# Kernel tuning notes

Measured on AMD Instinct MI355X. Metric: run time of the kernel, lower is better.

The kernel has to match this reference:

```python
import jax, jax.numpy as jnp
import numpy as np

DIM = 512
HEADS = 8
HEAD_DIM = DIM // HEADS
SCALE = HEAD_DIM ** -0.5


def setup_inputs() -> dict:
    key = jax.random.key(0)
    k1, k2, k3, k4, k5 = jax.random.split(key, 5)
    x = jax.random.normal(k1, (2, 4096, DIM), dtype=jnp.float32)
    # qkv Linear: weight [3*dim, dim], bias [3*dim]; proj: [dim, dim], [dim]
    w_qkv = jax.random.normal(k2, (3 * DIM, DIM), dtype=jnp.float32) * (DIM ** -0.5)
    b_qkv = jax.random.normal(k3, (3 * DIM,), dtype=jnp.float32) * 0.02
    w_proj = jax.random.normal(k4, (DIM, DIM), dtype=jnp.float32) * (DIM ** -0.5)
    b_proj = jax.random.normal(k5, (DIM,), dtype=jnp.float32) * 0.02
    return {"x": x, "w_qkv": w_qkv, "b_qkv": b_qkv, "w_proj": w_proj, "b_proj": b_proj}


def reference(x, w_qkv, b_qkv, w_proj, b_proj):
    B, N, C = x.shape
    qkv = x @ w_qkv.T + b_qkv  # [B, N, 3C]
    qkv = qkv.reshape(B, N, 3, HEADS, HEAD_DIM).transpose(2, 0, 3, 1, 4)  # [3,B,H,N,hd]
    q, k, v = qkv[0], qkv[1], qkv[2]
    attn = jnp.einsum('bhnd,bhmd->bhnm', q, k) * SCALE  # explicit NxN matrix
    attn = jax.nn.softmax(attn, axis=-1)
    out = jnp.einsum('bhnm,bhmd->bhnd', attn, v)  # [B,H,N,hd]
    out = out.transpose(0, 2, 1, 3).reshape(B, N, C)
    return out @ w_proj.T + b_proj
```

## Files before the change

kernel.cpp:

```cpp
#include <hip/hip_runtime.h>

typedef __bf16 bf16x8 __attribute__((ext_vector_type(8)));
typedef __bf16 bf16x4 __attribute__((ext_vector_type(4)));
typedef __bf16 bf16x2 __attribute__((ext_vector_type(2)));
typedef float  floatx4 __attribute__((ext_vector_type(4)));
typedef unsigned int uint32;
typedef uint32 uintx4 __attribute__((ext_vector_type(4)));

#define MFMA16(a,b,c) __builtin_amdgcn_mfma_f32_16x16x32_bf16(a,b,c,0,0,0)

constexpr int DIM  = 512;
constexpr int SEQ  = 4096;
constexpr int HD   = 64;
constexpr float QSCALE = 0.1803368801111244f;

static __device__ inline __bf16 f2bf(float f) {
    unsigned int u = __builtin_bit_cast(unsigned int, f);
    u += 0x7fffu + ((u >> 16) & 1u);
    return __builtin_bit_cast(__bf16, (unsigned short)(u >> 16));
}
#if __has_builtin(__builtin_amdgcn_cvt_pk_bf16_f32)
static __device__ inline bf16x2 pk2(float a, float b) {
    return __builtin_amdgcn_cvt_pk_bf16_f32(a, b);
}
#else
static __device__ inline bf16x2 pk2(float a, float b) {
    bf16x2 r; r[0] = f2bf(a); r[1] = f2bf(b); return r;
}
#endif
#if __has_builtin(__builtin_amdgcn_exp2f)
#define EXP2(x) __builtin_amdgcn_exp2f(x)
#else
#define EXP2(x) exp2f(x)
#endif
static __device__ inline bf16x8 cvt8(floatx4 lo, floatx4 hi) {
    uintx4 w;
    w[0] = __builtin_bit_cast(uint32, pk2(lo[0], lo[1]));
    w[1] = __builtin_bit_cast(uint32, pk2(lo[2], lo[3]));
    w[2] = __builtin_bit_cast(uint32, pk2(hi[0], hi[1]));
    w[3] = __builtin_bit_cast(uint32, pk2(hi[2], hi[3]));
    return __builtin_bit_cast(bf16x8, w);
}

static __device__ inline void gload16(const __bf16* g, __bf16* l) {
#if __has_builtin(__builtin_amdgcn_global_load_lds)
    __builtin_amdgcn_global_load_lds(
        (const __attribute__((address_space(1))) unsigned int*)g,
        (__attribute__((address_space(3))) unsigned int*)l, 16, 0, 0);
#else
    *(bf16x8*)(l + (threadIdx.x & 63)*8) = *(const bf16x8*)g;
#endif
}


__global__ __launch_bounds__(256)
void gemm_qkv(const float* __restrict__ X, const float* __restrict__ W,
              const float* __restrict__ bias,
              __bf16* __restrict__ Qb, __bf16* __restrict__ Kb, __bf16* __restrict__ Vb)
{
    __shared__ __bf16 As[128*32];
    __shared__ __bf16 Bs[128*32];
    const int tid  = threadIdx.x;
    const int lane = tid & 63;
    const int wave = tid >> 6;
    const int quad = lane >> 4;
    const int l16  = lane & 15;
    const int waveM = wave >> 1, waveN = wave & 1;
    const int mBase = blockIdx.x * 128;
    const int nBase = blockIdx.y * 128;
    const int which = nBase >> 9;

    floatx4 zero = {0.f, 0.f, 0.f, 0.f};
    floatx4 acc[4][4];
    for (int i = 0; i < 4; i++)
        for (int j = 0; j < 4; j++) acc[i][j] = zero;

    const int srow = tid >> 2;
    const int scol = (tid & 3) * 8;

    for (int k0 = 0; k0 < DIM; k0 += 32) {
        const float* xr0 = X + (size_t)(mBase + srow)      * DIM + k0 + scol;
        const float* xr1 = X + (size_t)(mBase + 64 + srow) * DIM + k0 + scol;
        const float* wr0 = W + (size_t)(nBase + srow)      * DIM + k0 + scol;
        const float* wr1 = W + (size_t)(nBase + 64 + srow) * DIM + k0 + scol;
        bf16x8 a0 = cvt8(*(const floatx4*)xr0, *(const floatx4*)(xr0 + 4));
        bf16x8 a1 = cvt8(*(const floatx4*)xr1, *(const floatx4*)(xr1 + 4));
        bf16x8 b0 = cvt8(*(const floatx4*)wr0, *(const floatx4*)(wr0 + 4));
        bf16x8 b1 = cvt8(*(const floatx4*)wr1, *(const floatx4*)(wr1 + 4));
        *(bf16x8*)&As[srow*32 + scol]      = a0;
        *(bf16x8*)&As[(64+srow)*32 + scol] = a1;
        *(bf16x8*)&Bs[srow*32 + scol]      = b0;
        *(bf16x8*)&Bs[(64+srow)*32 + scol] = b1;
        __syncthreads();
        bf16x8 af[4], bfr[4];
        for (int mi = 0; mi < 4; mi++)
            af[mi]  = *(const bf16x8*)&As[(waveM*64 + mi*16 + l16)*32 + quad*8];
        for (int ni = 0; ni < 4; ni++)
            bfr[ni] = *(const bf16x8*)&Bs[(waveN*64 + ni*16 + l16)*32 + quad*8];
        if (which == 2) {
            for (int mi = 0; mi < 4; mi++)
                for (int ni = 0; ni < 4; ni++)
                    acc[mi][ni] = MFMA16(af[mi], bfr[ni], acc[mi][ni]);
        } else {
            for (int mi = 0; mi < 4; mi++)
                for (int ni = 0; ni < 4; ni++)
                    acc[mi][ni] = MFMA16(bfr[ni], af[mi], acc[mi][ni]);
        }
        __syncthreads();
    }

    if (which == 2) {
        for (int ni = 0; ni < 4; ni++) {
            const int n = nBase + waveN*64 + ni*16 + l16;
            const float bv = bias[n];
            const int h = (n >> 6) & 7;
            const int d = n & 63;
            for (int mi = 0; mi < 4; mi++) {
                const int m0 = mBase + waveM*64 + mi*16 + quad*4;
                const int b  = m0 >> 12;
                const int s0 = m0 & 4095;
                const int bh = (b << 3) | h;
                bf16x4 v;
                for (int r = 0; r < 4; r++) v[r] = f2bf(acc[mi][ni][r] + bv);
                size_t off = (((((size_t)bh*128 + (s0 >> 5))*4 + (d >> 4))*64)
                              + ((s0 >> 2) & 3)*16 + (d & 15))*8 + ((s0 >> 4) & 1)*4;
                *(bf16x4*)&Vb[off] = v;
            }
        }
    } else {
        __bf16* dst = (which == 0) ? Qb : Kb;
        for (int ni = 0; ni < 4; ni++) {
            const int n0 = nBase + waveN*64 + ni*16 + quad*4;
            const floatx4 b4 = *(const floatx4*)&bias[n0];
            const int dfull = n0 & 511;
            const int h  = dfull >> 6;
            const int d0 = dfull & 63;
            const int lgrp = ((d0 >> 3) & 3)*16 + l16;
            const int half = d0 >> 5;
            const int slot = d0 & 7;
            for (int mi = 0; mi < 4; mi++) {
                const int m = mBase + waveM*64 + mi*16 + l16;
                const int b = m >> 12, s = m & 4095;
                const int bh = (b << 3) | h;
                bf16x4 v;
                for (int r = 0; r < 4; r++) {
                    float val = acc[mi][ni][r] + b4[r];
                    if (which == 0) val *= QSCALE;
                    v[r] = f2bf(val);
                }
                size_t off = ((((size_t)bh*256 + (s >> 4))*2 + half)*64 + lgrp)*8 + slot;
                *(bf16x4*)&dst[off] = v;
            }
        }
    }
}

__global__ __launch_bounds__(256, 3)
void attn_kernel(const __bf16* __restrict__ Qb, const __bf16* __restrict__ Kb,
                 const __bf16* __restrict__ Vb, __bf16* __restrict__ Ao)
{
    __shared__ __bf16 Ob[3][64*68];
    __shared__ float  Lb[4][64];
    const int tid  = threadIdx.x;
    const int lane = tid & 63;
    const int wave = tid >> 6;
    const int quad = lane >> 4;
    const int l16  = lane & 15;
    const int bh    = blockIdx.x;
    const int qBase = blockIdx.y * 64;

    const __bf16* qg = Qb + (size_t)bh*256*2*512;
    const __bf16* kg = Kb + (size_t)bh*256*2*512;
    const __bf16* vg = Vb + (size_t)bh*128*4*512;

    bf16x8 qf[4][2];
    for (int t = 0; t < 4; t++)
        for (int hb = 0; hb < 2; hb++)
            qf[t][hb] = *(const bf16x8*)(qg
                + ((size_t)((qBase >> 4) + t)*2 + hb)*512 + lane*8);

    floatx4 zero = {0.f, 0.f, 0.f, 0.f};
    floatx4 oacc[4][4];
    for (int t = 0; t < 4; t++)
        for (int od = 0; od < 4; od++) oacc[t][od] = zero;
    floatx4 Lt[4];
    for (int t = 0; t < 4; t++) Lt[t] = zero;

    bf16x8 ones;
    for (int j = 0; j < 8; j++) ones[j] = f2bf(1.0f);

    const int key_begin = wave * 1024;
    const __bf16* kptr = kg + (size_t)(key_begin >> 4)*1024 + lane*8;
    const __bf16* vptr = vg + (size_t)(key_begin >> 5)*2048 + lane*8;

    for (int c = 0; c < 32; ++c) {
        bf16x8 kb00 = *(const bf16x8*)(kptr);
        bf16x8 kb01 = *(const bf16x8*)(kptr + 512);
        bf16x8 kb10 = *(const bf16x8*)(kptr + 1024);
        bf16x8 kb11 = *(const bf16x8*)(kptr + 1536);
        bf16x8 vb0  = *(const bf16x8*)(vptr);
        bf16x8 vb1  = *(const bf16x8*)(vptr + 512);
        bf16x8 vb2  = *(const bf16x8*)(vptr + 1024);
        bf16x8 vb3  = *(const bf16x8*)(vptr + 1536);
        kptr += 2048;
        vptr += 2048;

        for (int t = 0; t < 4; t++) {
            floatx4 z0 = zero, z1 = zero;
            z0 = MFMA16(kb00, qf[t][0], z0);
            z0 = MFMA16(kb01, qf[t][1], z0);
            z1 = MFMA16(kb10, qf[t][0], z1);
            z1 = MFMA16(kb11, qf[t][1], z1);
            float e0[4], e1[4];
            for (int r = 0; r < 4; r++) { e0[r] = EXP2(z0[r]); e1[r] = EXP2(z1[r]); }
            uintx4 w;
            w[0] = __builtin_bit_cast(uint32, pk2(e0[0], e0[1]));
            w[1] = __builtin_bit_cast(uint32, pk2(e0[2], e0[3]));
            w[2] = __builtin_bit_cast(uint32, pk2(e1[0], e1[1]));
            w[3] = __builtin_bit_cast(uint32, pk2(e1[2], e1[3]));
            bf16x8 pb = __builtin_bit_cast(bf16x8, w);
            Lt[t] = MFMA16(ones, pb, Lt[t]);
            oacc[t][0] = MFMA16(vb0, pb, oacc[t][0]);
            oacc[t][1] = MFMA16(vb1, pb, oacc[t][1]);
            oacc[t][2] = MFMA16(vb2, pb, oacc[t][2]);
            oacc[t][3] = MFMA16(vb3, pb, oacc[t][3]);
        }
    }

    if (lane < 16)
        for (int t = 0; t < 4; t++) Lb[wave][t*16 + lane] = Lt[t][0];
    __syncthreads();
    float inv[4];
    for (int t = 0; t < 4; t++) {
        const int q = t*16 + l16;
        inv[t] = 1.0f / (Lb[0][q] + Lb[1][q] + Lb[2][q] + Lb[3][q]);
    }
    if (wave != 0) {
        for (int t = 0; t < 4; t++)
            for (int od = 0; od < 4; od++) {
                bf16x4 v;
                for (int r = 0; r < 4; r++) v[r] = f2bf(oacc[t][od][r] * inv[t]);
                *(bf16x4*)&Ob[wave-1][(t*16 + l16)*68 + od*16 + quad*4] = v;
            }
    }
    __syncthreads();
    if (wave == 0) {
        const int b = bh >> 3, h = bh & 7;
        for (int t = 0; t < 4; t++) {
            const int s = qBase + t*16 + l16;
            for (int od = 0; od < 4; od++) {
                bf16x4 o0 = *(const bf16x4*)&Ob[0][(t*16 + l16)*68 + od*16 + quad*4];
                bf16x4 o1 = *(const bf16x4*)&Ob[1][(t*16 + l16)*68 + od*16 + quad*4];
                bf16x4 o2 = *(const bf16x4*)&Ob[2][(t*16 + l16)*68 + od*16 + quad*4];
                bf16x4 v;
                for (int r = 0; r < 4; r++) {
                    float o = oacc[t][od][r] * inv[t] +
                              (float)o0[r] + (float)o1[r] + (float)o2[r];
                    v[r] = f2bf(o);
                }
                *(bf16x4*)&Ao[((size_t)(b*SEQ + s))*DIM + h*HD + od*16 + quad*4] = v;
            }
        }
    }
}

__global__ __launch_bounds__(256)
void gemm_proj(const __bf16* __restrict__ A, const float* __restrict__ W,
               const float* __restrict__ bias, float* __restrict__ Out)
{
    __shared__ __bf16 As[128*32];
    __shared__ __bf16 Bs[128*32];
    const int tid  = threadIdx.x;
    const int lane = tid & 63;
    const int wave = tid >> 6;
    const int quad = lane >> 4;
    const int l16  = lane & 15;
    const int waveM = wave >> 1, waveN = wave & 1;
    const int mBase = blockIdx.x * 128;
    const int nBase = blockIdx.y * 128;

    floatx4 zero = {0.f, 0.f, 0.f, 0.f};
    floatx4 acc[4][4];
    for (int i = 0; i < 4; i++)
        for (int j = 0; j < 4; j++) acc[i][j] = zero;

    const int srow = tid >> 2;
    const int scol = (tid & 3) * 8;
    const __bf16* gA0 = A + (size_t)(mBase + 32*wave + (lane >> 2))*DIM + (lane & 3)*8;
    __bf16* lA0 = &As[(32*wave)*32];
    __bf16* lA1 = &As[(32*wave + 16)*32];

    for (int k0 = 0; k0 < DIM; k0 += 32) {
        gload16(gA0 + k0,          lA0);
        gload16(gA0 + k0 + 16*DIM, lA1);
        const float* wr0 = W + (size_t)(nBase + srow)      * DIM + k0 + scol;
        const float* wr1 = W + (size_t)(nBase + 64 + srow) * DIM + k0 + scol;
        bf16x8 b0 = cvt8(*(const floatx4*)wr0, *(const floatx4*)(wr0 + 4));
        bf16x8 b1 = cvt8(*(const floatx4*)wr1, *(const floatx4*)(wr1 + 4));
        *(bf16x8*)&Bs[srow*32 + scol]      = b0;
        *(bf16x8*)&Bs[(64+srow)*32 + scol] = b1;
        __syncthreads();
        bf16x8 af[4], bfr[4];
        for (int mi = 0; mi < 4; mi++)
            af[mi]  = *(const bf16x8*)&As[(waveM*64 + mi*16 + l16)*32 + quad*8];
        for (int ni = 0; ni < 4; ni++)
            bfr[ni] = *(const bf16x8*)&Bs[(waveN*64 + ni*16 + l16)*32 + quad*8];
        for (int mi = 0; mi < 4; mi++)
            for (int ni = 0; ni < 4; ni++)
                acc[mi][ni] = MFMA16(af[mi], bfr[ni], acc[mi][ni]);
        __syncthreads();
    }

    for (int ni = 0; ni < 4; ni++) {
        const int n = nBase + waveN*64 + ni*16 + l16;
        const float bv = bias[n];
        for (int mi = 0; mi < 4; mi++) {
            const int m0 = mBase + waveM*64 + mi*16 + quad*4;
            for (int r = 0; r < 4; r++) {
                const int mm = m0 + r;
                Out[(size_t)mm*DIM + n] = acc[mi][ni][r] + bv;
            }
        }
    }
}

extern "C" void kernel_launch(void* const* d_in, const int* in_sizes, int n_in,
                              void* d_out, int out_size, void* d_ws, size_t ws_size,
                              hipStream_t stream) {
    const float* x      = (const float*)d_in[0];
    const float* w_qkv  = (const float*)d_in[1];
    const float* b_qkv  = (const float*)d_in[2];
    const float* w_proj = (const float*)d_in[3];
    const float* b_proj = (const float*)d_in[4];
    float* out = (float*)d_out;

    __bf16* ws  = (__bf16*)d_ws;
    const size_t PLANE = (size_t)16 * SEQ * HD;
    __bf16* Qbk = ws;
    __bf16* Kbk = ws + PLANE;
    __bf16* Vbk = ws + 2*PLANE;
    __bf16* Aob = ws + 3*PLANE;

    gemm_qkv<<<dim3(64, 12), 256, 0, stream>>>(x, w_qkv, b_qkv, Qbk, Kbk, Vbk);
    attn_kernel<<<dim3(16, 64), 256, 0, stream>>>(Qbk, Kbk, Vbk, Aob);
    gemm_proj<<<dim3(64, 4), 256, 0, stream>>>(Aob, w_proj, b_proj, out);
}
```

Before: 229.2 us.

## Double-buffer GEMM tiles, software-pipeline attention K/V loads, shrink proj tiles

The QKV GEMM now uses double-buffered LDS tiles, issuing the next k-slice's global loads before the current MFMAs and storing them afterwards, so each iteration needs one barrier instead of two. The attention kernel prefetches the next K/V chunk into registers while computing the current one, wraps the MFMA groups in s_setprio, and relaxes launch bounds from 3 to 2 waves per SIMD to leave room for the extra registers. The projection GEMM switches to 64x64 double-buffered tiles launched as a 128x8 grid to raise occupancy and parallelism. The cost is more register and LDS use per block, and lower occupancy in attention.

Result: faster. 214.5 us (-6.4%).

```diff
diff --git a/kernel.cpp b/kernel.cpp
--- a/kernel.cpp
+++ b/kernel.cpp
@@ -58,8 +58,8 @@
               const float* __restrict__ bias,
               __bf16* __restrict__ Qb, __bf16* __restrict__ Kb, __bf16* __restrict__ Vb)
 {
-    __shared__ __bf16 As[128*32];
-    __shared__ __bf16 Bs[128*32];
+    __shared__ __bf16 As[2][128*32];
+    __shared__ __bf16 Bs[2][128*32];
     const int tid  = threadIdx.x;
     const int lane = tid & 63;
     const int wave = tid >> 6;
@@ -78,25 +78,38 @@
     const int srow = tid >> 2;
     const int scol = (tid & 3) * 8;
 
-    for (int k0 = 0; k0 < DIM; k0 += 32) {
-        const float* xr0 = X + (size_t)(mBase + srow)      * DIM + k0 + scol;
-        const float* xr1 = X + (size_t)(mBase + 64 + srow) * DIM + k0 + scol;
-        const float* wr0 = W + (size_t)(nBase + srow)      * DIM + k0 + scol;
-        const float* wr1 = W + (size_t)(nBase + 64 + srow) * DIM + k0 + scol;
-        bf16x8 a0 = cvt8(*(const floatx4*)xr0, *(const floatx4*)(xr0 + 4));
-        bf16x8 a1 = cvt8(*(const floatx4*)xr1, *(const floatx4*)(xr1 + 4));
-        bf16x8 b0 = cvt8(*(const floatx4*)wr0, *(const floatx4*)(wr0 + 4));
-        bf16x8 b1 = cvt8(*(const floatx4*)wr1, *(const floatx4*)(wr1 + 4));
-        *(bf16x8*)&As[srow*32 + scol]      = a0;
-        *(bf16x8*)&As[(64+srow)*32 + scol] = a1;
-        *(bf16x8*)&Bs[srow*32 + scol]      = b0;
-        *(bf16x8*)&Bs[(64+srow)*32 + scol] = b1;
-        __syncthreads();
+    const float* xp0 = X + (size_t)(mBase + srow)      * DIM + scol;
+    const float* xp1 = X + (size_t)(mBase + 64 + srow) * DIM + scol;
+    const float* wp0 = W + (size_t)(nBase + srow)      * DIM + scol;
+    const float* wp1 = W + (size_t)(nBase + 64 + srow) * DIM + scol;
+
+    floatx4 r[8];
+    auto LOAD = [&](int k0) {
+        r[0] = *(const floatx4*)(xp0 + k0); r[1] = *(const floatx4*)(xp0 + k0 + 4);
+        r[2] = *(const floatx4*)(xp1 + k0); r[3] = *(const floatx4*)(xp1 + k0 + 4);
+        r[4] = *(const floatx4*)(wp0 + k0); r[5] = *(const floatx4*)(wp0 + k0 + 4);
+        r[6] = *(const floatx4*)(wp1 + k0); r[7] = *(const floatx4*)(wp1 + k0 + 4);
+    };
+    auto STORE = [&](int b) {
+        *(bf16x8*)&As[b][srow*32 + scol]      = cvt8(r[0], r[1]);
+        *(bf16x8*)&As[b][(64+srow)*32 + scol] = cvt8(r[2], r[3]);
+        *(bf16x8*)&Bs[b][srow*32 + scol]      = cvt8(r[4], r[5]);
+        *(bf16x8*)&Bs[b][(64+srow)*32 + scol] = cvt8(r[6], r[7]);
+    };
+
+    LOAD(0);
+    STORE(0);
+    __syncthreads();
+
+    for (int it = 0; it < 16; ++it) {
+        const int cur = it & 1;
+        if (it < 15) LOAD((it + 1) * 32);
+
         bf16x8 af[4], bfr[4];
         for (int mi = 0; mi < 4; mi++)
-            af[mi]  = *(const bf16x8*)&As[(waveM*64 + mi*16 + l16)*32 + quad*8];
+            af[mi]  = *(const bf16x8*)&As[cur][(waveM*64 + mi*16 + l16)*32 + quad*8];
         for (int ni = 0; ni < 4; ni++)
-            bfr[ni] = *(const bf16x8*)&Bs[(waveN*64 + ni*16 + l16)*32 + quad*8];
+            bfr[ni] = *(const bf16x8*)&Bs[cur][(waveN*64 + ni*16 + l16)*32 + quad*8];
         if (which == 2) {
             for (int mi = 0; mi < 4; mi++)
                 for (int ni = 0; ni < 4; ni++)
@@ -106,6 +119,7 @@
                 for (int ni = 0; ni < 4; ni++)
                     acc[mi][ni] = MFMA16(bfr[ni], af[mi], acc[mi][ni]);
         }
+        if (it < 15) STORE(cur ^ 1);
         __syncthreads();
     }
 
@@ -121,7 +135,7 @@
                 const int s0 = m0 & 4095;
                 const int bh = (b << 3) | h;
                 bf16x4 v;
-                for (int r = 0; r < 4; r++) v[r] = f2bf(acc[mi][ni][r] + bv);
+                for (int rr = 0; rr < 4; rr++) v[rr] = f2bf(acc[mi][ni][rr] + bv);
                 size_t off = (((((size_t)bh*128 + (s0 >> 5))*4 + (d >> 4))*64)
                               + ((s0 >> 2) & 3)*16 + (d & 15))*8 + ((s0 >> 4) & 1)*4;
                 *(bf16x4*)&Vb[off] = v;
@@ -143,10 +157,10 @@
                 const int b = m >> 12, s = m & 4095;
                 const int bh = (b << 3) | h;
                 bf16x4 v;
-                for (int r = 0; r < 4; r++) {
-                    float val = acc[mi][ni][r] + b4[r];
+                for (int rr = 0; rr < 4; rr++) {
+                    float val = acc[mi][ni][rr] + b4[rr];
                     if (which == 0) val *= QSCALE;
-                    v[r] = f2bf(val);
+                    v[rr] = f2bf(val);
                 }
                 size_t off = ((((size_t)bh*256 + (s >> 4))*2 + half)*64 + lgrp)*8 + slot;
                 *(bf16x4*)&dst[off] = v;
@@ -155,7 +169,7 @@
     }
 }
 
-__global__ __launch_bounds__(256, 3)
+__global__ __launch_bounds__(256, 2)
 void attn_kernel(const __bf16* __restrict__ Qb, const __bf16* __restrict__ Kb,
                  const __bf16* __restrict__ Vb, __bf16* __restrict__ Ao)
 {
@@ -189,42 +203,54 @@
     bf16x8 ones;
     for (int j = 0; j < 8; j++) ones[j] = f2bf(1.0f);
 
-    const int key_begin = wave * 1024;
-    const __bf16* kptr = kg + (size_t)(key_begin >> 4)*1024 + lane*8;
-    const __bf16* vptr = vg + (size_t)(key_begin >> 5)*2048 + lane*8;
-
-    for (int c = 0; c < 32; ++c) {
-        bf16x8 kb00 = *(const bf16x8*)(kptr);
-        bf16x8 kb01 = *(const bf16x8*)(kptr + 512);
-        bf16x8 kb10 = *(const bf16x8*)(kptr + 1024);
-        bf16x8 kb11 = *(const bf16x8*)(kptr + 1536);
-        bf16x8 vb0  = *(const bf16x8*)(vptr);
-        bf16x8 vb1  = *(const bf16x8*)(vptr + 512);
-        bf16x8 vb2  = *(const bf16x8*)(vptr + 1024);
-        bf16x8 vb3  = *(const bf16x8*)(vptr + 1536);
-        kptr += 2048;
-        vptr += 2048;
-
+    const int kvBase = wave * 32;
+
+    auto LOADKV = [&](int cc, bf16x8 (&kb)[4], bf16x8 (&vb)[4]) {
+        const __bf16* kp = kg + (size_t)(kvBase + cc)*2048 + lane*8;
+        const __bf16* vp = vg + (size_t)(kvBase + cc)*2048 + lane*8;
+        kb[0] = *(const bf16x8*)(kp);
+        kb[1] = *(const bf16x8*)(kp + 512);
+        kb[2] = *(const bf16x8*)(kp + 1024);
+        kb[3] = *(const bf16x8*)(kp + 1536);
+        vb[0] = *(const bf16x8*)(vp);
+        vb[1] = *(const bf16x8*)(vp + 512);
+        vb[2] = *(const bf16x8*)(vp + 1024);
+        vb[3] = *(const bf16x8*)(vp + 1536);
+    };
+    auto COMPUTE = [&](bf16x8 (&kb)[4], bf16x8 (&vb)[4]) {
         for (int t = 0; t < 4; t++) {
             floatx4 z0 = zero, z1 = zero;
-            z0 = MFMA16(kb00, qf[t][0], z0);
-            z0 = MFMA16(kb01, qf[t][1], z0);
-            z1 = MFMA16(kb10, qf[t][0], z1);
-            z1 = MFMA16(kb11, qf[t][1], z1);
+            __builtin_amdgcn_s_setprio(1);
+            z0 = MFMA16(kb[0], qf[t][0], z0);
+            z0 = MFMA16(kb[1], qf[t][1], z0);
+            z1 = MFMA16(kb[2], qf[t][0], z1);
+            z1 = MFMA16(kb[3], qf[t][1], z1);
+            __builtin_amdgcn_s_setprio(0);
             float e0[4], e1[4];
-            for (int r = 0; r < 4; r++) { e0[r] = EXP2(z0[r]); e1[r] = EXP2(z1[r]); }
+            for (int rr = 0; rr < 4; rr++) { e0[rr] = EXP2(z0[rr]); e1[rr] = EXP2(z1[rr]); }
             uintx4 w;
             w[0] = __builtin_bit_cast(uint32, pk2(e0[0], e0[1]));
             w[1] = __builtin_bit_cast(uint32, pk2(e0[2], e0[3]));
             w[2] = __builtin_bit_cast(uint32, pk2(e1[0], e1[1]));
             w[3] = __builtin_bit_cast(uint32, pk2(e1[2], e1[3]));
             bf16x8 pb = __builtin_bit_cast(bf16x8, w);
+            __builtin_amdgcn_s_setprio(1);
             Lt[t] = MFMA16(ones, pb, Lt[t]);
-            oacc[t][0] = MFMA16(vb0, pb, oacc[t][0]);
-            oacc[t][1] = MFMA16(vb1, pb, oacc[t][1]);
-            oacc[t][2] = MFMA16(vb2, pb, oacc[t][2]);
-            oacc[t][3] = MFMA16(vb3, pb, oacc[t][3]);
-        }
+            oacc[t][0] = MFMA16(vb[0], pb, oacc[t][0]);
+            oacc[t][1] = MFMA16(vb[1], pb, oacc[t][1]);
+            oacc[t][2] = MFMA16(vb[2], pb, oacc[t][2]);
+            oacc[t][3] = MFMA16(vb[3], pb, oacc[t][3]);
+            __builtin_amdgcn_s_setprio(0);
+        }
+    };
+
+    bf16x8 ka[4], va[4], kb2[4], vb2[4];
+    LOADKV(0, ka, va);
+    for (int c = 0; c < 32; c += 2) {
+        LOADKV(c + 1, kb2, vb2);
+        COMPUTE(ka, va);
+        if (c + 2 < 32) LOADKV(c + 2, ka, va);
+        COMPUTE(kb2, vb2);
     }
 
     if (lane < 16)
@@ -239,7 +265,7 @@
         for (int t = 0; t < 4; t++)
             for (int od = 0; od < 4; od++) {
                 bf16x4 v;
-                for (int r = 0; r < 4; r++) v[r] = f2bf(oacc[t][od][r] * inv[t]);
+                for (int rr = 0; rr < 4; rr++) v[rr] = f2bf(oacc[t][od][rr] * inv[t]);
                 *(bf16x4*)&Ob[wave-1][(t*16 + l16)*68 + od*16 + quad*4] = v;
             }
     }
@@ -253,10 +279,10 @@
                 bf16x4 o1 = *(const bf16x4*)&Ob[1][(t*16 + l16)*68 + od*16 + quad*4];
                 bf16x4 o2 = *(const bf16x4*)&Ob[2][(t*16 + l16)*68 + od*16 + quad*4];
                 bf16x4 v;
-                for (int r = 0; r < 4; r++) {
-                    float o = oacc[t][od][r] * inv[t] +
-                              (float)o0[r] + (float)o1[r] + (float)o2[r];
-                    v[r] = f2bf(o);
+                for (int rr = 0; rr < 4; rr++) {
+                    float o = oacc[t][od][rr] * inv[t] +
+                              (float)o0[rr] + (float)o1[rr] + (float)o2[rr];
+                    v[rr] = f2bf(o);
                 }
                 *(bf16x4*)&Ao[((size_t)(b*SEQ + s))*DIM + h*HD + od*16 + quad*4] = v;
             }
@@ -268,58 +294,62 @@
 void gemm_proj(const __bf16* __restrict__ A, const float* __restrict__ W,
                const float* __restrict__ bias, float* __restrict__ Out)
 {
-    __shared__ __bf16 As[128*32];
-    __shared__ __bf16 Bs[128*32];
+    __shared__ __bf16 As[2][64*32];
+    __shared__ __bf16 Bs[2][64*32];
     const int tid  = threadIdx.x;
     const int lane = tid & 63;
     const int wave = tid >> 6;
     const int quad = lane >> 4;
     const int l16  = lane & 15;
     const int waveM = wave >> 1, waveN = wave & 1;
-    const int mBase = blockIdx.x * 128;
-    const int nBase = blockIdx.y * 128;
+    const int mBase = blockIdx.x * 64;
+    const int nBase = blockIdx.y * 64;
 
     floatx4 zero = {0.f, 0.f, 0.f, 0.f};
-    floatx4 acc[4][4];
-    for (int i = 0; i < 4; i++)
-        for (int j = 0; j < 4; j++) acc[i][j] = zero;
+    floatx4 acc[2][2];
+    for (int i = 0; i < 2; i++)
+        for (int j = 0; j < 2; j++) acc[i][j] = zero;
 
     const int srow = tid >> 2;
     const int scol = (tid & 3) * 8;
-    const __bf16* gA0 = A + (size_t)(mBase + 32*wave + (lane >> 2))*DIM + (lane & 3)*8;
-    __bf16* lA0 = &As[(32*wave)*32];
-    __bf16* lA1 = &As[(32*wave + 16)*32];
-
-    for (int k0 = 0; k0 < DIM; k0 += 32) {
-        gload16(gA0 + k0,          lA0);
-        gload16(gA0 + k0 + 16*DIM, lA1);
-        const float* wr0 = W + (size_t)(nBase + srow)      * DIM + k0 + scol;
-        const float* wr1 = W + (size_t)(nBase + 64 + srow) * DIM + k0 + scol;
-        bf16x8 b0 = cvt8(*(const floatx4*)wr0, *(const floatx4*)(wr0 + 4));
-        bf16x8 b1 = cvt8(*(const floatx4*)wr1, *(const floatx4*)(wr1 + 4));
-        *(bf16x8*)&Bs[srow*32 + scol]      = b0;
-        *(bf16x8*)&Bs[(64+srow)*32 + scol] = b1;
+
+    const __bf16* gA = A + (size_t)(mBase + wave*16 + (lane >> 2))*DIM + (lane & 3)*8;
+    const float*  gW = W + (size_t)(nBase + srow)*DIM + scol;
+
+    floatx4 rw0, rw1;
+    gload16(gA, &As[0][wave*512]);
+    rw0 = *(const floatx4*)(gW);
+    rw1 = *(const floatx4*)(gW + 4);
+    *(bf16x8*)&Bs[0][srow*32 + scol] = cvt8(rw0, rw1);
+    __syncthreads();
+
+    for (int it = 0; it < 16; ++it) {
+        const int cur = it & 1;
+        if (it < 15) {
+            gload16(gA + (it + 1)*32, &As[cur ^ 1][wave*512]);
+            rw0 = *(const floatx4*)(gW + (it + 1)*32);
+            rw1 = *(const floatx4*)(gW + (it + 1)*32 + 4);
+        }
+        bf16x8 af[2], bfr[2];
+        for (int mi = 0; mi < 2; mi++)
+            af[mi]  = *(const bf16x8*)&As[cur][(waveM*32 + mi*16 + l16)*32 + quad*8];
+        for (int ni = 0; ni < 2; ni++)
+            bfr[ni] = *(const bf16x8*)&Bs[cur][(waveN*32 + ni*16 + l16)*32 + quad*8];
+        for (int mi = 0; mi < 2; mi++)
+            for (int ni = 0; ni < 2; ni++)
+                acc[mi][ni] = MFMA16(af[mi], bfr[ni], acc[mi][ni]);
+        if (it < 15)
+            *(bf16x8*)&Bs[cur ^ 1][srow*32 + scol] = cvt8(rw0, rw1);
         __syncthreads();
-        bf16x8 af[4], bfr[4];
-        for (int mi = 0; mi < 4; mi++)
-            af[mi]  = *(const bf16x8*)&As[(waveM*64 + mi*16 + l16)*32 + quad*8];
-        for (int ni = 0; ni < 4; ni++)
-            bfr[ni] = *(const bf16x8*)&Bs[(waveN*64 + ni*16 + l16)*32 + quad*8];
-        for (int mi = 0; mi < 4; mi++)
-            for (int ni = 0; ni < 4; ni++)
-                acc[mi][ni] = MFMA16(af[mi], bfr[ni], acc[mi][ni]);
-        __syncthreads();
-    }
-
-    for (int ni = 0; ni < 4; ni++) {
-        const int n = nBase + waveN*64 + ni*16 + l16;
+    }
+
+    for (int ni = 0; ni < 2; ni++) {
+        const int n = nBase + waveN*32 + ni*16 + l16;
         const float bv = bias[n];
-        for (int mi = 0; mi < 4; mi++) {
-            const int m0 = mBase + waveM*64 + mi*16 + quad*4;
-            for (int r = 0; r < 4; r++) {
-                const int mm = m0 + r;
-                Out[(size_t)mm*DIM + n] = acc[mi][ni][r] + bv;
-            }
+        for (int mi = 0; mi < 2; mi++) {
+            const int m0 = mBase + waveM*32 + mi*16 + quad*4;
+            for (int rr = 0; rr < 4; rr++)
+                Out[(size_t)(m0 + rr)*DIM + n] = acc[mi][ni][rr] + bv;
         }
     }
 }
@@ -343,5 +373,5 @@
 
     gemm_qkv<<<dim3(64, 12), 256, 0, stream>>>(x, w_qkv, b_qkv, Qbk, Kbk, Vbk);
     attn_kernel<<<dim3(16, 64), 256, 0, stream>>>(Qbk, Kbk, Vbk, Aob);
-    gemm_proj<<<dim3(64, 4), 256, 0, stream>>>(Aob, w_proj, b_proj, out);
-}
+    gemm_proj<<<dim3(128, 8), 256, 0, stream>>>(Aob, w_proj, b_proj, out);
+}
```
